# Performance work log

Measured on AMD Instinct MI355X. Metric: run time of the kernel, lower is better.

Reference implementation:

```python
import jax, jax.numpy as jnp
import numpy as np

B, FEAT, H, V = 512, 2048, 512, 100
STEPS = 200  # TEXT_MAX_LEN - 1
SOS = 0      # char2idx['<SOS>']


def setup_inputs() -> dict:
    key = jax.random.key(0)
    ks = jax.random.split(key, 8)
    s = 0.02  # small init keeps tanh/sigmoid in a sane range over 200 steps
    return {
        "feat": jax.random.normal(ks[0], (B, FEAT), jnp.float32),
        "w_hp": jax.random.normal(ks[1], (FEAT, H), jnp.float32) * s,
        "b_hp": jnp.zeros((H,), jnp.float32),
        "embed": jax.random.normal(ks[2], (V, H), jnp.float32) * s,
        "w_ih": jax.random.normal(ks[3], (3 * H, H), jnp.float32) * s,
        "w_hh": jax.random.normal(ks[4], (3 * H, H), jnp.float32) * s,
        "b_ih": jnp.zeros((3 * H,), jnp.float32),
        "b_hh": jnp.zeros((3 * H,), jnp.float32),
        "w_proj": jax.random.normal(ks[5], (H, V), jnp.float32) * s,
        "b_proj": jnp.zeros((V,), jnp.float32),
    }


def _gru_cell(x, h, w_ih, w_hh, b_ih, b_hh):
    # PyTorch GRU cell: gates ordered (reset, update, new)
    gi = x @ w_ih.T + b_ih            # [B, 3H]
    gh = h @ w_hh.T + b_hh            # [B, 3H]
    i_r, i_z, i_n = jnp.split(gi, 3, axis=-1)
    h_r, h_z, h_n = jnp.split(gh, 3, axis=-1)
    r = jax.nn.sigmoid(i_r + h_r)
    z = jax.nn.sigmoid(i_z + h_z)
    n = jnp.tanh(i_n + r * h_n)
    return (1.0 - z) * n + z * h      # new hidden = output


def reference(feat, w_hp, b_hp, embed, w_ih, w_hh, b_ih, b_hh, w_proj, b_proj):
    # hidden init = hidden_proj(resnet pooled feature)  -> [B, H]
    h0 = feat @ w_hp + b_hp
    # first input = embedding of <SOS>, broadcast over batch
    x0 = jnp.broadcast_to(embed[SOS], (feat.shape[0], embed.shape[1]))

    def step(carry, _):
        h, x = carry
        h_new = _gru_cell(x, h, w_ih, w_hh, b_ih, b_hh)
        # output feeds back as next step's input (out -> inp)
        return (h_new, h_new), h_new

    _, outs = jax.lax.scan(step, (h0, x0), None, length=STEPS)  # [T, B, H]
    res = jnp.transpose(outs, (1, 0, 2))                        # [B, T, H]
    logits = res @ w_proj + b_proj                              # [B, T, V]
    return jnp.transpose(logits, (0, 2, 1))                     # [B, V, T]
```

## Files before the change

kernel.cpp:

```cpp
#include <hip/hip_runtime.h>

#define Bsz  512
#define FEAT 2048
#define Hd   512
#define Vd   100
#define Td   200
#define Gd   2048

typedef __bf16 bf16;
typedef __bf16 bf16x8 __attribute__((ext_vector_type(8)));
typedef float  f32x4  __attribute__((ext_vector_type(4)));

__device__ bf16  g_hbuf[Td + 1][Bsz][Hd];
__device__ bf16  g_hping[2][Bsz][Hd];
__device__ bf16  g_wt0[Gd][Hd];
__device__ bf16  g_wt1[Gd][Hd];
__device__ float g_bias0[Gd];
__device__ float g_bias1[Gd];
__device__ bf16  g_featbf[Bsz][FEAT];
__device__ bf16  g_whpt[Hd][FEAT];
__device__ bf16  g_wprojt[112][Hd];
__device__ float g_gi0[3 * Hd];
__device__ unsigned g_flags[32][8];
__device__ unsigned g_dbar[32][16];
__device__ unsigned g_xcd[256];

template <int OFF>
__device__ __forceinline__ bf16x8 ld_b16x8_cohere(const void* p) {
  bf16x8 r;
  asm volatile("global_load_dwordx4 %0, %1, off offset:%2 sc0 sc1"
               : "=&v"(r) : "v"(p), "i"(OFF) : "memory");
  return r;
}
template <int OFF>
__device__ __forceinline__ bf16x8 ld_b16x8_l2(const void* p) {
  bf16x8 r;
  asm volatile("global_load_dwordx4 %0, %1, off offset:%2 sc1"
               : "=&v"(r) : "v"(p), "i"(OFF) : "memory");
  return r;
}
template <int OFF>
__device__ __forceinline__ void st_u16_cohere(void* p, unsigned short v) {
  asm volatile("global_store_short %0, %1, off offset:%2 sc0 sc1"
               :: "v"(p), "v"(v), "i"(OFF) : "memory");
}
__device__ __forceinline__ void st_u32_cohere(void* p, unsigned v) {
  asm volatile("global_store_dword %0, %1, off sc0 sc1" :: "v"(p), "v"(v) : "memory");
}
__device__ __forceinline__ unsigned ld_u32_cohere(const void* p) {
  unsigned r;
  asm volatile("global_load_dword %0, %1, off sc0 sc1\n\ts_waitcnt vmcnt(0)"
               : "=&v"(r) : "v"(p) : "memory");
  return r;
}
__device__ __forceinline__ unsigned atomic_rd(unsigned* p) {
  unsigned r;
  asm volatile("global_atomic_add %0, %1, %2, off sc0\n\ts_waitcnt vmcnt(0)"
               : "=&v"(r) : "v"(p), "v"(0u) : "memory");
  return r;
}
__device__ __forceinline__ void atomic_inc(unsigned* p) {
  asm volatile("global_atomic_add %0, %1, off" :: "v"(p), "v"(1u) : "memory");
}
__device__ __forceinline__ void wait_vm0() { asm volatile("s_waitcnt vmcnt(0)" ::: "memory"); }
__device__ __forceinline__ void wait_vm8() { asm volatile("s_waitcnt vmcnt(8)" ::: "memory"); }

#define LDA16(arr, base) do {                                                   \
  arr[0]  = ld_b16x8_cohere<0>(base);   arr[1]  = ld_b16x8_cohere<64>(base);    \
  arr[2]  = ld_b16x8_cohere<128>(base); arr[3]  = ld_b16x8_cohere<192>(base);   \
  arr[4]  = ld_b16x8_cohere<256>(base); arr[5]  = ld_b16x8_cohere<320>(base);   \
  arr[6]  = ld_b16x8_cohere<384>(base); arr[7]  = ld_b16x8_cohere<448>(base);   \
  arr[8]  = ld_b16x8_cohere<512>(base); arr[9]  = ld_b16x8_cohere<576>(base);   \
  arr[10] = ld_b16x8_cohere<640>(base); arr[11] = ld_b16x8_cohere<704>(base);   \
  arr[12] = ld_b16x8_cohere<768>(base); arr[13] = ld_b16x8_cohere<832>(base);   \
  arr[14] = ld_b16x8_cohere<896>(base); arr[15] = ld_b16x8_cohere<960>(base);   \
} while (0)

#define LDA16_L2(arr, base) do {                                                \
  arr[0]  = ld_b16x8_l2<0>(base);   arr[1]  = ld_b16x8_l2<64>(base);            \
  arr[2]  = ld_b16x8_l2<128>(base); arr[3]  = ld_b16x8_l2<192>(base);           \
  arr[4]  = ld_b16x8_l2<256>(base); arr[5]  = ld_b16x8_l2<320>(base);           \
  arr[6]  = ld_b16x8_l2<384>(base); arr[7]  = ld_b16x8_l2<448>(base);           \
  arr[8]  = ld_b16x8_l2<512>(base); arr[9]  = ld_b16x8_l2<576>(base);           \
  arr[10] = ld_b16x8_l2<640>(base); arr[11] = ld_b16x8_l2<704>(base);           \
  arr[12] = ld_b16x8_l2<768>(base); arr[13] = ld_b16x8_l2<832>(base);           \
  arr[14] = ld_b16x8_l2<896>(base); arr[15] = ld_b16x8_l2<960>(base);           \
} while (0)

__device__ __forceinline__ float sigmoidf_(float x) {
  x = fminf(fmaxf(x, -30.f), 30.f);
  return 1.f / (1.f + __expf(-x));
}
__device__ __forceinline__ float tanhf_(float x) {
  x = fminf(fmaxf(x, -15.f), 15.f);
  float e = __expf(2.f * x);
  return (e - 1.f) / (e + 1.f);
}

__device__ __forceinline__ void group_barrier(int rg, int cg, unsigned phase) {
  wait_vm0();
  __syncthreads();
  if (threadIdx.x == 0) st_u32_cohere(&g_flags[rg][cg], phase);
  if (threadIdx.x < 64) {
    const unsigned* fp = &g_flags[rg][threadIdx.x & 7];
    while (ld_u32_cohere(fp) < phase) __builtin_amdgcn_s_sleep(1);
  }
  __syncthreads();
}


__global__ void k_conv_feat(const float* feat) {
  int i = blockIdx.x * 256 + threadIdx.x;
  if (i < Bsz * FEAT) ((bf16*)g_featbf)[i] = (bf16)feat[i];
  if (blockIdx.x == 0) {
    ((unsigned*)g_flags)[threadIdx.x] = 0u;
    ((unsigned*)g_dbar)[threadIdx.x] = 0u;
    ((unsigned*)g_dbar)[256 + threadIdx.x] = 0u;
    g_xcd[threadIdx.x] = 0xffffffffu;
  }
}

__global__ void k_gi0(const float* embed, const float* w_ih, const float* b_ih) {
  int j = blockIdx.x;
  const float* wr = w_ih + (size_t)j * Hd;
  float s = 0.f;
  for (int k = threadIdx.x; k < Hd; k += 64) s += embed[k] * wr[k];
#pragma unroll
  for (int off = 32; off > 0; off >>= 1) s += __shfl_down(s, off);
  if (threadIdx.x == 0) g_gi0[j] = s + b_ih[j];
}

__global__ void k_build_wt1(const float* w_ih, const float* w_hh,
                            const float* b_ih, const float* b_hh) {
  int c = blockIdx.x;
  int j = (c >> 6) * 16 + (c & 15);
  int f = (c >> 4) & 3;
  const float* s1 = nullptr; const float* s2 = nullptr; float bias;
  if (f == 0)      { s1 = w_ih + (size_t)j * Hd;            s2 = w_hh + (size_t)j * Hd;            bias = b_ih[j] + b_hh[j]; }
  else if (f == 1) { s1 = w_ih + (size_t)(Hd + j) * Hd;     s2 = w_hh + (size_t)(Hd + j) * Hd;     bias = b_ih[Hd + j] + b_hh[Hd + j]; }
  else if (f == 2) { s1 = w_ih + (size_t)(2 * Hd + j) * Hd;                                        bias = b_ih[2 * Hd + j]; }
  else             { s1 = w_hh + (size_t)(2 * Hd + j) * Hd;                                        bias = b_hh[2 * Hd + j]; }
  for (int k = threadIdx.x; k < Hd; k += 256) {
    float v = s1[k] + (s2 ? s2[k] : 0.f);
    g_wt1[c][k] = (bf16)v;
  }
  if (threadIdx.x == 0) g_bias1[c] = bias;
}

__global__ void k_build_wt0(const float* w_hh, const float* b_hh) {
  int c = blockIdx.x;
  int j = (c >> 6) * 16 + (c & 15);
  int f = (c >> 4) & 3;
  const float* s1 = nullptr; float bias;
  if (f == 0)      { s1 = w_hh + (size_t)j * Hd;            bias = g_gi0[j] + b_hh[j]; }
  else if (f == 1) { s1 = w_hh + (size_t)(Hd + j) * Hd;     bias = g_gi0[Hd + j] + b_hh[Hd + j]; }
  else if (f == 2) {                                        bias = g_gi0[2 * Hd + j]; }
  else             { s1 = w_hh + (size_t)(2 * Hd + j) * Hd; bias = b_hh[2 * Hd + j]; }
  for (int k = threadIdx.x; k < Hd; k += 256)
    g_wt0[c][k] = (bf16)(s1 ? s1[k] : 0.f);
  if (threadIdx.x == 0) g_bias0[c] = bias;
}

__global__ void k_build_whpt(const float* w_hp) {
  int n = blockIdx.x;
  for (int k = threadIdx.x; k < FEAT; k += 256)
    g_whpt[n][k] = (bf16)w_hp[(size_t)k * Hd + n];
}

__global__ void k_build_wprojt(const float* w_proj) {
  int v = blockIdx.x;
  for (int k = threadIdx.x; k < Hd; k += 256)
    g_wprojt[v][k] = (bf16)(v < Vd ? w_proj[(size_t)k * Vd + v] : 0.f);
}

__global__ __launch_bounds__(256, 1) void k_gru_seq(const float* b_hp) {
  const int bid = blockIdx.x;
  const int rg = (bid & 7) * 4 + ((bid >> 3) & 3);
  const int cg = bid >> 5;
  const int w = threadIdx.x >> 6, l = threadIdx.x & 63;
  const int m = l & 15;
  const int ksub = (l >> 4) * 8;
  const int colb = (cg * 4 + w) * 64;
  const int arow = rg * 16 + m;
  const int srow = rg * 16 + (l >> 4) * 4;
  const int hcol = (cg * 4 + w) * 16 + m;
  __shared__ int s_fast;

  bf16x8 Bw[64];
#pragma unroll
  for (int f = 0; f < 4; f++)
#pragma unroll
    for (int k0 = 0; k0 < 16; k0++)
      Bw[f * 16 + k0] = *(const bf16x8*)&g_wt1[colb + f * 16 + m][k0 * 32 + ksub];

  float b0v[4], b1v[4];
#pragma unroll
  for (int f = 0; f < 4; f++) {
    b0v[f] = g_bias0[colb + f * 16 + m];
    b1v[f] = g_bias1[colb + f * 16 + m];
  }

  unsigned xcc;
  asm volatile("s_getreg_b32 %0, hwreg(HW_REG_XCC_ID)" : "=s"(xcc));
  if (threadIdx.x == 0) st_u32_cohere(&g_xcd[bid], xcc);
  group_barrier(rg, cg, 1u);
  if (threadIdx.x < 64) {
    int c = threadIdx.x & 7;
    unsigned peer = ld_u32_cohere(&g_xcd[(rg >> 2) + ((rg & 3) << 3) + (c << 5)]);
    unsigned long long bal = __ballot(peer == xcc);
    if (threadIdx.x == 0) s_fast = ((bal & 0xffull) == 0xffull) ? 1 : 0;
  }
  __syncthreads();
  const bool fast = (s_fast != 0);

  float hcarry[4];
  {
    f32x4 acc = {0.f, 0.f, 0.f, 0.f};
#pragma unroll 4
    for (int k0 = 0; k0 < FEAT; k0 += 32) {
      bf16x8 a = *(const bf16x8*)&g_featbf[arow][k0 + ksub];
      bf16x8 b = *(const bf16x8*)&g_whpt[hcol][k0 + ksub];
      acc = __builtin_amdgcn_mfma_f32_16x16x32_bf16(a, b, acc, 0, 0, 0);
    }
    float bhp = b_hp[hcol];
    unsigned short us[4];
#pragma unroll
    for (int i = 0; i < 4; i++) {
      bf16 hv = (bf16)(acc[i] + bhp);
      hcarry[i] = (float)hv;
      us[i] = __builtin_bit_cast(unsigned short, hv);
    }
    if (fast) {
      bf16* pp = &g_hping[0][srow][hcol];
#pragma unroll
      for (int i = 0; i < 4; i++) pp[i * Hd] = __builtin_bit_cast(bf16, us[i]);
    } else {
      char* pc = (char*)&g_hbuf[0][srow][hcol];
      st_u16_cohere<0>(pc, us[0]);    st_u16_cohere<1024>(pc, us[1]);
      st_u16_cohere<2048>(pc, us[2]); st_u16_cohere<3072>(pc, us[3]);
    }
  }

  if (fast) {
    unsigned* cnt = &g_dbar[rg][0];
    wait_vm0();
    __syncthreads();
    if (threadIdx.x == 0) {
      atomic_inc(cnt);
      while (atomic_rd(cnt) < 8u) { }
    }
    __syncthreads();

    for (int t = 0; t < Td; t++) {
      bf16x8 a[16];
      const char* Ap = (const char*)&g_hping[t & 1][arow][ksub];
      LDA16_L2(a, Ap);

      f32x4 acc[4], acc2[4];
#pragma unroll
      for (int f = 0; f < 4; f++) {
        float bv = (t == 0) ? b0v[f] : b1v[f];
        acc[f]  = (f32x4){bv, bv, bv, bv};
        acc2[f] = (f32x4){0.f, 0.f, 0.f, 0.f};
      }
      wait_vm8(); __builtin_amdgcn_sched_barrier(0);
      if (t == 0) {
#pragma unroll
        for (int k0 = 0; k0 < 8; k0++)
#pragma unroll
          for (int f = 0; f < 4; f++) {
            bf16x8 b = *(const bf16x8*)&g_wt0[colb + f * 16 + m][k0 * 32 + ksub];
            acc[f] = __builtin_amdgcn_mfma_f32_16x16x32_bf16(a[k0], b, acc[f], 0, 0, 0);
          }
        wait_vm0(); __builtin_amdgcn_sched_barrier(0);
#pragma unroll
        for (int k0 = 8; k0 < 16; k0++)
#pragma unroll
          for (int f = 0; f < 4; f++) {
            bf16x8 b = *(const bf16x8*)&g_wt0[colb + f * 16 + m][k0 * 32 + ksub];
            acc2[f] = __builtin_amdgcn_mfma_f32_16x16x32_bf16(a[k0], b, acc2[f], 0, 0, 0);
          }
      } else {
#pragma unroll
        for (int k0 = 0; k0 < 8; k0++)
#pragma unroll
          for (int f = 0; f < 4; f++)
            acc[f] = __builtin_amdgcn_mfma_f32_16x16x32_bf16(a[k0], Bw[f * 16 + k0], acc[f], 0, 0, 0);
        wait_vm0(); __builtin_amdgcn_sched_barrier(0);
#pragma unroll
        for (int k0 = 8; k0 < 16; k0++)
#pragma unroll
          for (int f = 0; f < 4; f++)
            acc2[f] = __builtin_amdgcn_mfma_f32_16x16x32_bf16(a[k0], Bw[f * 16 + k0], acc2[f], 0, 0, 0);
      }

      bf16 hv4[4];
      bf16* pp = &g_hping[(t + 1) & 1][srow][hcol];
#pragma unroll
      for (int i = 0; i < 4; i++) {
        float r = sigmoidf_(acc[0][i] + acc2[0][i]);
        float z = sigmoidf_(acc[1][i] + acc2[1][i]);
        float n = tanhf_((acc[2][i] + acc2[2][i]) + r * (acc[3][i] + acc2[3][i]));
        float hn = (1.f - z) * n + z * hcarry[i];
        bf16 hv = (bf16)hn;
        hcarry[i] = (float)hv;
        hv4[i] = hv;
        pp[i * Hd] = hv;
      }
      wait_vm0();

      bf16* ph = &g_hbuf[t + 1][srow][hcol];
#pragma unroll
      for (int i = 0; i < 4; i++) ph[i * Hd] = hv4[i];

      if (t < Td - 1) {
        __syncthreads();
        if (threadIdx.x == 0) {
          atomic_inc(cnt);
          unsigned tgt = 8u * (unsigned)(t + 2);
          while (atomic_rd(cnt) < tgt) { }
        }
        __syncthreads();
      }
    }
  } else {
    group_barrier(rg, cg, 2u);
    for (int t = 0; t < Td; t++) {
      bf16x8 a[16];
      const char* Ap = (const char*)&g_hbuf[t][arow][ksub];
      LDA16(a, Ap);

      f32x4 acc[4];
#pragma unroll
      for (int f = 0; f < 4; f++) {
        float bv = (t == 0) ? b0v[f] : b1v[f];
        acc[f] = (f32x4){bv, bv, bv, bv};
      }
      if (t == 0) {
        wait_vm0(); __builtin_amdgcn_sched_barrier(0);
#pragma unroll
        for (int k0 = 0; k0 < 16; k0++)
#pragma unroll
          for (int f = 0; f < 4; f++) {
            bf16x8 b = *(const bf16x8*)&g_wt0[colb + f * 16 + m][k0 * 32 + ksub];
            acc[f] = __builtin_amdgcn_mfma_f32_16x16x32_bf16(a[k0], b, acc[f], 0, 0, 0);
          }
      } else {
        wait_vm8(); __builtin_amdgcn_sched_barrier(0);
#pragma unroll
        for (int k0 = 0; k0 < 8; k0++)
#pragma unroll
          for (int f = 0; f < 4; f++)
            acc[f] = __builtin_amdgcn_mfma_f32_16x16x32_bf16(a[k0], Bw[f * 16 + k0], acc[f], 0, 0, 0);
        wait_vm0(); __builtin_amdgcn_sched_barrier(0);
#pragma unroll
        for (int k0 = 8; k0 < 16; k0++)
#pragma unroll
          for (int f = 0; f < 4; f++)
            acc[f] = __builtin_amdgcn_mfma_f32_16x16x32_bf16(a[k0], Bw[f * 16 + k0], acc[f], 0, 0, 0);
      }

      char* pb = (char*)&g_hbuf[t + 1][srow][hcol];
      unsigned short us[4];
#pragma unroll
      for (int i = 0; i < 4; i++) {
        float r = sigmoidf_(acc[0][i]);
        float z = sigmoidf_(acc[1][i]);
        float n = tanhf_(acc[2][i] + r * acc[3][i]);
        float hn = (1.f - z) * n + z * hcarry[i];
        bf16 hv = (bf16)hn;
        hcarry[i] = (float)hv;
        us[i] = __builtin_bit_cast(unsigned short, hv);
      }
      st_u16_cohere<0>(pb, us[0]);    st_u16_cohere<1024>(pb, us[1]);
      st_u16_cohere<2048>(pb, us[2]); st_u16_cohere<3072>(pb, us[3]);

      if (t < Td - 1) group_barrier(rg, cg, (unsigned)(t + 3));
    }
  }
  wait_vm0();
}

__global__ __launch_bounds__(256) void k_proj(const float* b_proj, float* out) {
  int b = blockIdx.x;
  int w = threadIdx.x >> 6, l = threadIdx.x & 63;
  int tt = blockIdx.y * 4 + w;
  if (tt > 12) return;
  int m = l & 15, ksub = (l >> 4) * 8;
  int tcol = tt * 16 + m;
  int trow = (tcol < Td ? tcol : Td - 1) + 1;

  f32x4 acc[7];
#pragma unroll
  for (int f = 0; f < 7; f++)
#pragma unroll
    for (int i = 0; i < 4; i++) {
      int v = f * 16 + (l >> 4) * 4 + i;
      acc[f][i] = (v < Vd) ? b_proj[v] : 0.f;
    }

  bf16x8 bb[16];
  const bf16* Bp = &g_hbuf[trow][b][ksub];
#pragma unroll
  for (int k0 = 0; k0 < 16; k0++) bb[k0] = *(const bf16x8*)(Bp + k0 * 32);

#pragma unroll
  for (int k0 = 0; k0 < 16; k0++)
#pragma unroll
    for (int f = 0; f < 7; f++) {
      bf16x8 afrag = *(const bf16x8*)&g_wprojt[f * 16 + m][k0 * 32 + ksub];
      acc[f] = __builtin_amdgcn_mfma_f32_16x16x32_bf16(afrag, bb[k0], acc[f], 0, 0, 0);
    }

  if (tcol < Td) {
#pragma unroll
    for (int f = 0; f < 7; f++)
#pragma unroll
      for (int i = 0; i < 4; i++) {
        int v = f * 16 + (l >> 4) * 4 + i;
        if (v < Vd) out[((size_t)b * Vd + v) * Td + tcol] = acc[f][i];
      }
  }
}

extern "C" void kernel_launch(void* const* d_in, const int* in_sizes, int n_in,
                              void* d_out, int out_size, void* d_ws, size_t ws_size,
                              hipStream_t stream) {
  const float* feat   = (const float*)d_in[0];
  const float* w_hp   = (const float*)d_in[1];
  const float* b_hp   = (const float*)d_in[2];
  const float* embed  = (const float*)d_in[3];
  const float* w_ih   = (const float*)d_in[4];
  const float* w_hh   = (const float*)d_in[5];
  const float* b_ih   = (const float*)d_in[6];
  const float* b_hh   = (const float*)d_in[7];
  const float* w_proj = (const float*)d_in[8];
  const float* b_proj = (const float*)d_in[9];
  float* out = (float*)d_out;

  hipLaunchKernelGGL(k_conv_feat, dim3((Bsz * FEAT) / 256), dim3(256), 0, stream, feat);
  hipLaunchKernelGGL(k_gi0, dim3(3 * Hd), dim3(64), 0, stream, embed, w_ih, b_ih);
  hipLaunchKernelGGL(k_build_wt1, dim3(Gd), dim3(256), 0, stream, w_ih, w_hh, b_ih, b_hh);
  hipLaunchKernelGGL(k_build_wt0, dim3(Gd), dim3(256), 0, stream, w_hh, b_hh);
  hipLaunchKernelGGL(k_build_whpt, dim3(Hd), dim3(256), 0, stream, w_hp);
  hipLaunchKernelGGL(k_build_wprojt, dim3(112), dim3(256), 0, stream, w_proj);
  hipLaunchKernelGGL(k_gru_seq, dim3(256), dim3(256), 0, stream, b_hp);
  hipLaunchKernelGGL(k_proj, dim3(Bsz, 4), dim3(256), 0, stream, b_proj, out);
}
```

Before: 954.4 us.

## Replace block barriers with per-wave counters and batch history writes via 8-slot staging ring

The fast path now uses an 8-deep staging ring of hidden states instead of a 2-slot ping-pong buffer. Each wave signals its own arrival on the group counter, and only wave 0 spins on it; the other waves wait on a shared-memory release flag instead of two __syncthreads per step. The scattered per-step 2-byte stores into the full history buffer are dropped. Every 8 steps the staged states are copied into the history with wide 16-byte loads and stores. This is meant to cut barrier and store overhead on the serial recurrence critical path, at the cost of extra staging memory, periodic copy work, and subtler memory-ordering correctness.

```diff
diff --git a/kernel.cpp b/kernel.cpp
--- a/kernel.cpp
+++ b/kernel.cpp
@@ -12,7 +12,7 @@
 typedef float  f32x4  __attribute__((ext_vector_type(4)));
 
 __device__ bf16  g_hbuf[Td + 1][Bsz][Hd];
-__device__ bf16  g_hping[2][Bsz][Hd];
+__device__ bf16  g_hstage[8][Bsz][Hd];
 __device__ bf16  g_wt0[Gd][Hd];
 __device__ bf16  g_wt1[Gd][Hd];
 __device__ float g_bias0[Gd];
@@ -184,7 +184,9 @@
   const int arow = rg * 16 + m;
   const int srow = rg * 16 + (l >> 4) * 4;
   const int hcol = (cg * 4 + w) * 16 + m;
+  const int hbase = (cg * 4 + w) * 16;
   __shared__ int s_fast;
+  __shared__ int s_rel;
 
   bf16x8 Bw[64];
 #pragma unroll
@@ -202,7 +204,7 @@
 
   unsigned xcc;
   asm volatile("s_getreg_b32 %0, hwreg(HW_REG_XCC_ID)" : "=s"(xcc));
-  if (threadIdx.x == 0) st_u32_cohere(&g_xcd[bid], xcc);
+  if (threadIdx.x == 0) { st_u32_cohere(&g_xcd[bid], xcc); s_rel = 0; }
   group_barrier(rg, cg, 1u);
   if (threadIdx.x < 64) {
     int c = threadIdx.x & 7;
@@ -231,7 +233,7 @@
       us[i] = __builtin_bit_cast(unsigned short, hv);
     }
     if (fast) {
-      bf16* pp = &g_hping[0][srow][hcol];
+      bf16* pp = &g_hstage[0][srow][hcol];
 #pragma unroll
       for (int i = 0; i < 4; i++) pp[i * Hd] = __builtin_bit_cast(bf16, us[i]);
     } else {
@@ -244,16 +246,21 @@
   if (fast) {
     unsigned* cnt = &g_dbar[rg][0];
     wait_vm0();
-    __syncthreads();
-    if (threadIdx.x == 0) {
-      atomic_inc(cnt);
-      while (atomic_rd(cnt) < 8u) { }
-    }
-    __syncthreads();
+    if (l == 0) atomic_inc(cnt);
 
     for (int t = 0; t < Td; t++) {
+      const int tgt = 32 * (t + 1);
+      if (w == 0) {
+        if (l == 0) {
+          while ((int)atomic_rd(cnt) < tgt) { }
+          __hip_atomic_store(&s_rel, t + 1, __ATOMIC_RELEASE, __HIP_MEMORY_SCOPE_WORKGROUP);
+        }
+      } else {
+        while (__hip_atomic_load(&s_rel, __ATOMIC_ACQUIRE, __HIP_MEMORY_SCOPE_WORKGROUP) < t + 1) { }
+      }
+
       bf16x8 a[16];
-      const char* Ap = (const char*)&g_hping[t & 1][arow][ksub];
+      const char* Ap = (const char*)&g_hstage[t & 7][arow][ksub];
       LDA16_L2(a, Ap);
 
       f32x4 acc[4], acc2[4];
@@ -294,8 +301,7 @@
             acc2[f] = __builtin_amdgcn_mfma_f32_16x16x32_bf16(a[k0], Bw[f * 16 + k0], acc2[f], 0, 0, 0);
       }
 
-      bf16 hv4[4];
-      bf16* pp = &g_hping[(t + 1) & 1][srow][hcol];
+      bf16* pp = &g_hstage[(t + 1) & 7][srow][hcol];
 #pragma unroll
       for (int i = 0; i < 4; i++) {
         float r = sigmoidf_(acc[0][i] + acc2[0][i]);
@@ -304,23 +310,26 @@
         float hn = (1.f - z) * n + z * hcarry[i];
         bf16 hv = (bf16)hn;
         hcarry[i] = (float)hv;
-        hv4[i] = hv;
         pp[i * Hd] = hv;
       }
       wait_vm0();
-
-      bf16* ph = &g_hbuf[t + 1][srow][hcol];
-#pragma unroll
-      for (int i = 0; i < 4; i++) ph[i * Hd] = hv4[i];
-
-      if (t < Td - 1) {
-        __syncthreads();
-        if (threadIdx.x == 0) {
-          atomic_inc(cnt);
-          unsigned tgt = 8u * (unsigned)(t + 2);
-          while (atomic_rd(cnt) < tgt) { }
-        }
-        __syncthreads();
+      if (l == 0) atomic_inc(cnt);
+
+      if ((t & 7) == 7) {
+        const int s = l >> 3;
+        const int v = (t + 1) - (((t + 1) - s) & 7);
+        const int r0 = rg * 16 + (l & 7) * 2;
+        const char* sp = (const char*)&g_hstage[s][r0][hbase];
+        char* dp = (char*)&g_hbuf[v][r0][hbase];
+        bf16x8 x0 = ld_b16x8_l2<0>(sp);
+        bf16x8 x1 = ld_b16x8_l2<16>(sp);
+        bf16x8 x2 = ld_b16x8_l2<1024>(sp);
+        bf16x8 x3 = ld_b16x8_l2<1040>(sp);
+        wait_vm0(); __builtin_amdgcn_sched_barrier(0);
+        *(bf16x8*)(dp)        = x0;
+        *(bf16x8*)(dp + 16)   = x1;
+        *(bf16x8*)(dp + 1024) = x2;
+        *(bf16x8*)(dp + 1040) = x3;
       }
     }
   } else {
```

After: 979.2 us. 1.03x slower.
